# Optimization experiments

Measured on AMD Instinct MI355X. Metric: run time of the kernel, lower is better.

The kernel has to match this reference:

```python
import jax, jax.numpy as jnp
import numpy as np

EPS = 1e-5

def sparse_up_add(x, W, in_idx, out_idx, gamma, beta, skip):
    # x: [N_in, Cin]; W: [K, Cin, Cout]; in_idx/out_idx: [K, P]; skip: [N_out, Cout]
    n_out, c_out = skip.shape
    g = x[in_idx]                                   # [K, P, Cin] gather
    contrib = jnp.einsum('kpi,kio->kpo', g, W)      # [K, P, Cout] GEMM
    out = jnp.zeros((n_out, c_out), x.dtype)
    out = out.at[out_idx.reshape(-1)].add(contrib.reshape(-1, c_out))  # scatter-add
    # BatchNorm1d (training mode: batch stats over active voxels)
    mean = out.mean(axis=0)
    var = out.var(axis=0)
    y = (out - mean) * jax.lax.rsqrt(var + EPS) * gamma + beta
    return y + skip


def setup_inputs() -> dict:
    key = jax.random.key(0)
    ks = jax.random.split(key, 20)
    N3, N2, N1, N0 = 40000, 160000, 640000, 2560000
    C3, C2, C1 = 128, 64, 32
    K = 9
    d = {}
    d['x3'] = jax.random.normal(ks[0], (N3, C3), jnp.float32)
    d['skip3'] = jax.random.normal(ks[1], (N2, C2), jnp.float32)
    d['skip2'] = jax.random.normal(ks[2], (N1, C1), jnp.float32)
    d['skip1'] = jax.random.normal(ks[3], (N0, C1), jnp.float32)
    d['W3'] = jax.random.normal(ks[4], (K, C3, C2), jnp.float32) * (1.0 / np.sqrt(C3 * K))
    d['W2'] = jax.random.normal(ks[5], (K, C2, C1), jnp.float32) * (1.0 / np.sqrt(C2 * K))
    d['W1'] = jax.random.normal(ks[6], (K, C1, C1), jnp.float32) * (1.0 / np.sqrt(C1 * K))
    d['gamma3'] = jnp.ones((C2,), jnp.float32); d['beta3'] = jnp.zeros((C2,), jnp.float32)
    d['gamma2'] = jnp.ones((C1,), jnp.float32); d['beta2'] = jnp.zeros((C1,), jnp.float32)
    d['gamma1'] = jnp.ones((C1,), jnp.float32); d['beta1'] = jnp.zeros((C1,), jnp.float32)
    d['in_idx3'] = jax.random.randint(ks[7], (K, N3), 0, N3, jnp.int32)
    d['out_idx3'] = jax.random.randint(ks[8], (K, N3), 0, N2, jnp.int32)
    d['in_idx2'] = jax.random.randint(ks[9], (K, N2), 0, N2, jnp.int32)
    d['out_idx2'] = jax.random.randint(ks[10], (K, N2), 0, N1, jnp.int32)
    d['in_idx1'] = jax.random.randint(ks[11], (K, N1), 0, N1, jnp.int32)
    d['out_idx1'] = jax.random.randint(ks[12], (K, N1), 0, N0, jnp.int32)
    return d


def reference(x3, skip3, skip2, skip1, W3, W2, W1, gamma3, beta3, gamma2, beta2, gamma1, beta1,
              in_idx3, out_idx3, in_idx2, out_idx2, in_idx1, out_idx1):
    x = sparse_up_add(x3, W3, in_idx3, out_idx3, gamma3, beta3, skip3)  # up_3
    x = sparse_up_add(x, W2, in_idx2, out_idx2, gamma2, beta2, skip2)   # up_2
    x = sparse_up_add(x, W1, in_idx1, out_idx1, gamma1, beta1, skip1)   # up_1
    return x
```

## Files before the change

kernel.cpp:

```cpp
#include <hip/hip_runtime.h>

#define EPS 1e-5f

template <int CIN, int COUT, int RPB>
__global__ __launch_bounds__(256) void scatter_gemm_wreg(
    const float* __restrict__ x, const float* __restrict__ W,
    const int* __restrict__ in_idx, const int* __restrict__ out_idx,
    float* __restrict__ out, int P)
{
    const int GROUPS = 256 / COUT;
    const int k = blockIdx.y;
    const int o = threadIdx.x % COUT;
    const int g = threadIdx.x / COUT;

    float wcol[CIN];
    const float* __restrict__ Wk = W + (size_t)k * CIN * COUT + o;
#pragma unroll
    for (int i = 0; i < CIN; ++i) wcol[i] = Wk[(size_t)i * COUT];

    const int p0 = blockIdx.x * RPB;
    const int p1 = (p0 + RPB < P) ? (p0 + RPB) : P;
    const int rbase = k * P;

    for (int p = p0 + g; p < p1; p += GROUPS) {
        const int r = rbase + p;
        const int in   = in_idx[r];
        const int orow = out_idx[r];
        const float4* __restrict__ xr4 = (const float4*)(x + (size_t)in * CIN);
        float acc = 0.f;
#pragma unroll
        for (int i4 = 0; i4 < CIN / 4; ++i4) {
            const float4 xv = xr4[i4];
            acc = fmaf(xv.x, wcol[4 * i4 + 0], acc);
            acc = fmaf(xv.y, wcol[4 * i4 + 1], acc);
            acc = fmaf(xv.z, wcol[4 * i4 + 2], acc);
            acc = fmaf(xv.w, wcol[4 * i4 + 3], acc);
        }
        atomicAdd(&out[(size_t)orow * COUT + o], acc);
    }
}

template <int CIN, int RPB>
__global__ __launch_bounds__(256) void scatter_gemm_h2(
    const float* __restrict__ x, const float* __restrict__ W,
    const int* __restrict__ in_idx, const int* __restrict__ out_idx,
    float* __restrict__ out, int P)
{
    const int COUT = 32;
    const int HC = CIN / 2;
    const int WAVES = 256 / 64;
    const int k = blockIdx.y;
    const int lane = threadIdx.x & 63;
    const int w = threadIdx.x >> 6;
    const int o = lane & 31;
    const int h = lane >> 5;

    float wcol[HC];
    const float* __restrict__ Wk =
        W + (size_t)k * CIN * COUT + (size_t)h * HC * COUT + o;
#pragma unroll
    for (int i = 0; i < HC; ++i) wcol[i] = Wk[(size_t)i * COUT];

    const int p0 = blockIdx.x * RPB;
    const int p1 = (p0 + RPB < P) ? (p0 + RPB) : P;
    const int rbase = k * P;

    for (int p = p0 + w; p < p1; p += WAVES) {
        const int r = rbase + p;
        const int in   = in_idx[r];
        const int orow = out_idx[r];
        const float4* __restrict__ xr4 =
            (const float4*)(x + (size_t)in * CIN + h * HC);
        float acc = 0.f;
#pragma unroll
        for (int i4 = 0; i4 < HC / 4; ++i4) {
            const float4 xv = xr4[i4];
            acc = fmaf(xv.x, wcol[4 * i4 + 0], acc);
            acc = fmaf(xv.y, wcol[4 * i4 + 1], acc);
            acc = fmaf(xv.z, wcol[4 * i4 + 2], acc);
            acc = fmaf(xv.w, wcol[4 * i4 + 3], acc);
        }
        acc += __shfl_xor(acc, 32);
        if (h == 0) atomicAdd(&out[(size_t)orow * COUT + o], acc);
    }
}

template <int RPB>
__global__ __launch_bounds__(256) void scatter_gemm_l3_h2(
    const float* __restrict__ x, const float* __restrict__ W,
    const int* __restrict__ in_idx, const int* __restrict__ out_idx,
    float* __restrict__ out, int P)
{
    const int CIN = 128, COUT = 64;
    const int lane2 = threadIdx.x & 127;
    const int rg = threadIdx.x >> 7;
    const int o = lane2 & 63;
    const int h = lane2 >> 6;
    const int k = blockIdx.y;

    float wcol[64];
    const float* __restrict__ Wk =
        W + (size_t)k * CIN * COUT + (size_t)h * 64 * COUT + o;
#pragma unroll
    for (int i = 0; i < 64; ++i) wcol[i] = Wk[(size_t)i * COUT];

    __shared__ float part[2][64];

    const int p0 = blockIdx.x * RPB;
    const int rbase = k * P;

    for (int it = 0; it < RPB / 2; ++it) {
        const int p = p0 + it * 2 + rg;
        const int r = rbase + p;
        const int in   = in_idx[r];
        const int orow = out_idx[r];
        const float4* __restrict__ xr4 =
            (const float4*)(x + (size_t)in * CIN + h * 64);
        float acc = 0.f;
#pragma unroll
        for (int i4 = 0; i4 < 16; ++i4) {
            const float4 xv = xr4[i4];
            acc = fmaf(xv.x, wcol[4 * i4 + 0], acc);
            acc = fmaf(xv.y, wcol[4 * i4 + 1], acc);
            acc = fmaf(xv.z, wcol[4 * i4 + 2], acc);
            acc = fmaf(xv.w, wcol[4 * i4 + 3], acc);
        }
        if (h == 1) part[rg][o] = acc;
        __syncthreads();
        if (h == 0) {
            acc += part[rg][o];
            atomicAdd(&out[(size_t)orow * COUT + o], acc);
        }
        __syncthreads();
    }
}

template <int COUT>
__global__ __launch_bounds__(256) void reduce_stats(
    const float* __restrict__ out, float* __restrict__ stats, int n_rows)
{
    const int RPP = 256 / COUT;
    int c = threadIdx.x % COUT;
    float s = 0.f, ss = 0.f;
    int g = threadIdx.x / COUT;
    for (long long row = (long long)blockIdx.x * RPP + g; row < n_rows;
         row += (long long)gridDim.x * RPP) {
        float v = out[row * COUT + c];
        s += v;
        ss += v * v;
    }
    __shared__ float sh_s[256];
    __shared__ float sh_ss[256];
    sh_s[threadIdx.x] = s;
    sh_ss[threadIdx.x] = ss;
    __syncthreads();
    for (int off = 128; off >= COUT; off >>= 1) {
        if (threadIdx.x < off) {
            sh_s[threadIdx.x] += sh_s[threadIdx.x + off];
            sh_ss[threadIdx.x] += sh_ss[threadIdx.x + off];
        }
        __syncthreads();
    }
    if (threadIdx.x < COUT) {
        atomicAdd(&stats[c], sh_s[c]);
        atomicAdd(&stats[COUT + c], sh_ss[c]);
    }
}

template <int COUT>
__global__ __launch_bounds__(256) void bn_skip(
    float* __restrict__ out, const float* __restrict__ skip,
    const float* __restrict__ gamma, const float* __restrict__ beta,
    const float* __restrict__ stats, int n_rows)
{
    const int C4 = COUT / 4;
    long long idx = (long long)blockIdx.x * blockDim.x + threadIdx.x;
    long long total = (long long)n_rows * C4;
    if (idx >= total) return;
    int c4 = (int)(idx % C4);
    float4 v = ((const float4*)out)[idx];
    float4 sk = ((const float4*)skip)[idx];
    float inv_n = 1.f / (float)n_rows;
    float r[4] = {v.x, v.y, v.z, v.w};
    float skv[4] = {sk.x, sk.y, sk.z, sk.w};
#pragma unroll
    for (int j = 0; j < 4; ++j) {
        int c = c4 * 4 + j;
        float mean = stats[c] * inv_n;
        float var = stats[COUT + c] * inv_n - mean * mean;
        float scale = rsqrtf(var + EPS) * gamma[c];
        r[j] = (r[j] - mean) * scale + beta[c] + skv[j];
    }
    float4 res = {r[0], r[1], r[2], r[3]};
    ((float4*)out)[idx] = res;
}

extern "C" void kernel_launch(void* const* d_in, const int* in_sizes, int n_in,
                              void* d_out, int out_size, void* d_ws, size_t ws_size,
                              hipStream_t stream) {
    const float* x3    = (const float*)d_in[0];
    const float* skip3 = (const float*)d_in[1];
    const float* skip2 = (const float*)d_in[2];
    const float* skip1 = (const float*)d_in[3];
    const float* W3    = (const float*)d_in[4];
    const float* W2    = (const float*)d_in[5];
    const float* W1    = (const float*)d_in[6];
    const float* gamma3 = (const float*)d_in[7];
    const float* beta3  = (const float*)d_in[8];
    const float* gamma2 = (const float*)d_in[9];
    const float* beta2  = (const float*)d_in[10];
    const float* gamma1 = (const float*)d_in[11];
    const float* beta1  = (const float*)d_in[12];
    const int* in_idx3  = (const int*)d_in[13];
    const int* out_idx3 = (const int*)d_in[14];
    const int* in_idx2  = (const int*)d_in[15];
    const int* out_idx2 = (const int*)d_in[16];
    const int* in_idx1  = (const int*)d_in[17];
    const int* out_idx1 = (const int*)d_in[18];

    const int N3 = 40000, N2 = 160000, N1 = 640000, N0 = 2560000;
    const int K = 9;

    float* buf3  = (float*)d_ws;
    float* buf2  = buf3 + (size_t)N2 * 64;
    float* stats = buf2 + (size_t)N1 * 32;

    float* outp = (float*)d_out;

    hipMemsetAsync(buf3, 0, (size_t)N2 * 64 * sizeof(float), stream);
    hipMemsetAsync(stats, 0, 128 * sizeof(float), stream);
    {
        const int RPB = 16;
        dim3 grid(N3 / RPB, K);
        scatter_gemm_l3_h2<RPB><<<grid, 256, 0, stream>>>(
            x3, W3, in_idx3, out_idx3, buf3, N3);
    }
    reduce_stats<64><<<1024, 256, 0, stream>>>(buf3, stats, N2);
    {
        long long tot = (long long)N2 * (64 / 4);
        bn_skip<64><<<(int)((tot + 255) / 256), 256, 0, stream>>>(
            buf3, skip3, gamma3, beta3, stats, N2);
    }

    hipMemsetAsync(buf2, 0, (size_t)N1 * 32 * sizeof(float), stream);
    hipMemsetAsync(stats, 0, 128 * sizeof(float), stream);
    {
        const int RPB = 32;
        dim3 grid(N2 / RPB, K);
        scatter_gemm_h2<64, RPB><<<grid, 256, 0, stream>>>(
            buf3, W2, in_idx2, out_idx2, buf2, N2);
    }
    reduce_stats<32><<<2048, 256, 0, stream>>>(buf2, stats, N1);
    {
        long long tot = (long long)N1 * (32 / 4);
        bn_skip<32><<<(int)((tot + 255) / 256), 256, 0, stream>>>(
            buf2, skip2, gamma2, beta2, stats, N1);
    }

    hipMemsetAsync(outp, 0, (size_t)N0 * 32 * sizeof(float), stream);
    hipMemsetAsync(stats, 0, 128 * sizeof(float), stream);
    {
        const int RPB = 64;
        dim3 grid((N1 + RPB - 1) / RPB, K);
        scatter_gemm_wreg<32, 32, RPB><<<grid, 256, 0, stream>>>(
            buf2, W1, in_idx1, out_idx1, outp, N1);
    }
    reduce_stats<32><<<4096, 256, 0, stream>>>(outp, stats, N0);
    {
        long long tot = (long long)N0 * (32 / 4);
        bn_skip<32><<<(int)((tot + 255) / 256), 256, 0, stream>>>(
            outp, skip1, gamma1, beta1, stats, N0);
    }
}
```

Before: 2.947 ms.

## Unroll scatter-GEMM rows by two, split accumulators, drop LDS sync in layer 3

```diff
diff --git a/kernel.cpp b/kernel.cpp
--- a/kernel.cpp
+++ b/kernel.cpp
@@ -3,12 +3,13 @@
 #define EPS 1e-5f
 
 template <int CIN, int COUT, int RPB>
-__global__ __launch_bounds__(256) void scatter_gemm_wreg(
+__global__ __launch_bounds__(256, 8) void scatter_gemm_wreg2(
     const float* __restrict__ x, const float* __restrict__ W,
     const int* __restrict__ in_idx, const int* __restrict__ out_idx,
     float* __restrict__ out, int P)
 {
     const int GROUPS = 256 / COUT;
+    const int ITERS = RPB / GROUPS;
     const int k = blockIdx.y;
     const int o = threadIdx.x % COUT;
     const int g = threadIdx.x / COUT;
@@ -18,37 +19,47 @@
 #pragma unroll
     for (int i = 0; i < CIN; ++i) wcol[i] = Wk[(size_t)i * COUT];
 
-    const int p0 = blockIdx.x * RPB;
-    const int p1 = (p0 + RPB < P) ? (p0 + RPB) : P;
-    const int rbase = k * P;
-
-    for (int p = p0 + g; p < p1; p += GROUPS) {
-        const int r = rbase + p;
-        const int in   = in_idx[r];
-        const int orow = out_idx[r];
-        const float4* __restrict__ xr4 = (const float4*)(x + (size_t)in * CIN);
-        float acc = 0.f;
+    const int rbase = k * P + blockIdx.x * RPB + g;
+
+    for (int it = 0; it < ITERS; it += 2) {
+        const int r0 = rbase + it * GROUPS;
+        const int r1 = r0 + GROUPS;
+        const int in0 = in_idx[r0];
+        const int or0 = out_idx[r0];
+        const int in1 = in_idx[r1];
+        const int or1 = out_idx[r1];
+        const float4* __restrict__ a4 = (const float4*)(x + (size_t)in0 * CIN);
+        const float4* __restrict__ b4 = (const float4*)(x + (size_t)in1 * CIN);
+        float aa0 = 0.f, aa1 = 0.f, aa2 = 0.f, aa3 = 0.f;
+        float ba0 = 0.f, ba1 = 0.f, ba2 = 0.f, ba3 = 0.f;
 #pragma unroll
         for (int i4 = 0; i4 < CIN / 4; ++i4) {
-            const float4 xv = xr4[i4];
-            acc = fmaf(xv.x, wcol[4 * i4 + 0], acc);
-            acc = fmaf(xv.y, wcol[4 * i4 + 1], acc);
-            acc = fmaf(xv.z, wcol[4 * i4 + 2], acc);
-            acc = fmaf(xv.w, wcol[4 * i4 + 3], acc);
-        }
-        atomicAdd(&out[(size_t)orow * COUT + o], acc);
+            const float4 av = a4[i4];
+            const float4 bv = b4[i4];
+            aa0 = fmaf(av.x, wcol[4 * i4 + 0], aa0);
+            aa1 = fmaf(av.y, wcol[4 * i4 + 1], aa1);
+            aa2 = fmaf(av.z, wcol[4 * i4 + 2], aa2);
+            aa3 = fmaf(av.w, wcol[4 * i4 + 3], aa3);
+            ba0 = fmaf(bv.x, wcol[4 * i4 + 0], ba0);
+            ba1 = fmaf(bv.y, wcol[4 * i4 + 1], ba1);
+            ba2 = fmaf(bv.z, wcol[4 * i4 + 2], ba2);
+            ba3 = fmaf(bv.w, wcol[4 * i4 + 3], ba3);
+        }
+        atomicAdd(&out[(size_t)or0 * COUT + o], (aa0 + aa1) + (aa2 + aa3));
+        atomicAdd(&out[(size_t)or1 * COUT + o], (ba0 + ba1) + (ba2 + ba3));
     }
 }
 
 template <int CIN, int RPB>
-__global__ __launch_bounds__(256) void scatter_gemm_h2(
+__global__ __launch_bounds__(256, 8) void scatter_gemm_h2u(
     const float* __restrict__ x, const float* __restrict__ W,
     const int* __restrict__ in_idx, const int* __restrict__ out_idx,
     float* __restrict__ out, int P)
 {
     const int COUT = 32;
     const int HC = CIN / 2;
-    const int WAVES = 256 / 64;
+    const int WAVES = 4;
+    const int ITERS = RPB / WAVES;
     const int k = blockIdx.y;
     const int lane = threadIdx.x & 63;
     const int w = threadIdx.x >> 6;
@@ -61,77 +72,82 @@
 #pragma unroll
     for (int i = 0; i < HC; ++i) wcol[i] = Wk[(size_t)i * COUT];
 
-    const int p0 = blockIdx.x * RPB;
-    const int p1 = (p0 + RPB < P) ? (p0 + RPB) : P;
-    const int rbase = k * P;
-
-    for (int p = p0 + w; p < p1; p += WAVES) {
-        const int r = rbase + p;
-        const int in   = in_idx[r];
-        const int orow = out_idx[r];
-        const float4* __restrict__ xr4 =
-            (const float4*)(x + (size_t)in * CIN + h * HC);
-        float acc = 0.f;
+    const int rbase = k * P + blockIdx.x * RPB + w;
+
+    for (int it = 0; it < ITERS; it += 2) {
+        const int r0 = rbase + it * WAVES;
+        const int r1 = r0 + WAVES;
+        const int in0 = in_idx[r0];
+        const int or0 = out_idx[r0];
+        const int in1 = in_idx[r1];
+        const int or1 = out_idx[r1];
+        const float4* __restrict__ a4 =
+            (const float4*)(x + (size_t)in0 * CIN + h * HC);
+        const float4* __restrict__ b4 =
+            (const float4*)(x + (size_t)in1 * CIN + h * HC);
+        float aa0 = 0.f, aa1 = 0.f;
+        float ba0 = 0.f, ba1 = 0.f;
 #pragma unroll
         for (int i4 = 0; i4 < HC / 4; ++i4) {
-            const float4 xv = xr4[i4];
-            acc = fmaf(xv.x, wcol[4 * i4 + 0], acc);
-            acc = fmaf(xv.y, wcol[4 * i4 + 1], acc);
-            acc = fmaf(xv.z, wcol[4 * i4 + 2], acc);
-            acc = fmaf(xv.w, wcol[4 * i4 + 3], acc);
-        }
-        acc += __shfl_xor(acc, 32);
-        if (h == 0) atomicAdd(&out[(size_t)orow * COUT + o], acc);
+            const float4 av = a4[i4];
+            const float4 bv = b4[i4];
+            aa0 = fmaf(av.x, wcol[4 * i4 + 0], aa0);
+            aa1 = fmaf(av.y, wcol[4 * i4 + 1], aa1);
+            aa0 = fmaf(av.z, wcol[4 * i4 + 2], aa0);
+            aa1 = fmaf(av.w, wcol[4 * i4 + 3], aa1);
+            ba0 = fmaf(bv.x, wcol[4 * i4 + 0], ba0);
+            ba1 = fmaf(bv.y, wcol[4 * i4 + 1], ba1);
+            ba0 = fmaf(bv.z, wcol[4 * i4 + 2], ba0);
+            ba1 = fmaf(bv.w, wcol[4 * i4 + 3], ba1);
+        }
+        float acc0 = aa0 + aa1;
+        float acc1 = ba0 + ba1;
+        acc0 += __shfl_xor(acc0, 32);
+        acc1 += __shfl_xor(acc1, 32);
+        if (h == 0) {
+            atomicAdd(&out[(size_t)or0 * COUT + o], acc0);
+            atomicAdd(&out[(size_t)or1 * COUT + o], acc1);
+        }
     }
 }
 
 template <int RPB>
-__global__ __launch_bounds__(256) void scatter_gemm_l3_h2(
+__global__ __launch_bounds__(256, 4) void scatter_gemm_l3w(
     const float* __restrict__ x, const float* __restrict__ W,
     const int* __restrict__ in_idx, const int* __restrict__ out_idx,
     float* __restrict__ out, int P)
 {
     const int CIN = 128, COUT = 64;
-    const int lane2 = threadIdx.x & 127;
-    const int rg = threadIdx.x >> 7;
-    const int o = lane2 & 63;
-    const int h = lane2 >> 6;
+    const int w = threadIdx.x >> 6;
+    const int o = threadIdx.x & 63;
+    const int rp = w >> 1;
+    const int h = w & 1;
     const int k = blockIdx.y;
 
     float wcol[64];
     const float* __restrict__ Wk =
-        W + (size_t)k * CIN * COUT + (size_t)h * 64 * COUT + o;
+        W + (size_t)k * CIN * COUT + (size_t)(h * 64) * COUT + o;
 #pragma unroll
     for (int i = 0; i < 64; ++i) wcol[i] = Wk[(size_t)i * COUT];
 
-    __shared__ float part[2][64];
-
-    const int p0 = blockIdx.x * RPB;
-    const int rbase = k * P;
+    const int rbase = k * P + blockIdx.x * RPB + rp;
 
     for (int it = 0; it < RPB / 2; ++it) {
-        const int p = p0 + it * 2 + rg;
-        const int r = rbase + p;
-        const int in   = in_idx[r];
+        const int r = rbase + it * 2;
+        const int in = in_idx[r];
         const int orow = out_idx[r];
         const float4* __restrict__ xr4 =
             (const float4*)(x + (size_t)in * CIN + h * 64);
-        float acc = 0.f;
+        float a0 = 0.f, a1 = 0.f, a2 = 0.f, a3 = 0.f;
 #pragma unroll
         for (int i4 = 0; i4 < 16; ++i4) {
             const float4 xv = xr4[i4];
-            acc = fmaf(xv.x, wcol[4 * i4 + 0], acc);
-            acc = fmaf(xv.y, wcol[4 * i4 + 1], acc);
-            acc = fmaf(xv.z, wcol[4 * i4 + 2], acc);
-            acc = fmaf(xv.w, wcol[4 * i4 + 3], acc);
-        }
-        if (h == 1) part[rg][o] = acc;
-        __syncthreads();
-        if (h == 0) {
-            acc += part[rg][o];
-            atomicAdd(&out[(size_t)orow * COUT + o], acc);
-        }
-        __syncthreads();
+            a0 = fmaf(xv.x, wcol[4 * i4 + 0], a0);
+            a1 = fmaf(xv.y, wcol[4 * i4 + 1], a1);
+            a2 = fmaf(xv.z, wcol[4 * i4 + 2], a2);
+            a3 = fmaf(xv.w, wcol[4 * i4 + 3], a3);
+        }
+        atomicAdd(&out[(size_t)orow * COUT + o], (a0 + a1) + (a2 + a3));
     }
 }
 
@@ -232,7 +248,7 @@
     {
         const int RPB = 16;
         dim3 grid(N3 / RPB, K);
-        scatter_gemm_l3_h2<RPB><<<grid, 256, 0, stream>>>(
+        scatter_gemm_l3w<RPB><<<grid, 256, 0, stream>>>(
             x3, W3, in_idx3, out_idx3, buf3, N3);
     }
     reduce_stats<64><<<1024, 256, 0, stream>>>(buf3, stats, N2);
@@ -247,7 +263,7 @@
     {
         const int RPB = 32;
         dim3 grid(N2 / RPB, K);
-        scatter_gemm_h2<64, RPB><<<grid, 256, 0, stream>>>(
+        scatter_gemm_h2u<64, RPB><<<grid, 256, 0, stream>>>(
             buf3, W2, in_idx2, out_idx2, buf2, N2);
     }
     reduce_stats<32><<<2048, 256, 0, stream>>>(buf2, stats, N1);
@@ -261,8 +277,8 @@
     hipMemsetAsync(stats, 0, 128 * sizeof(float), stream);
     {
         const int RPB = 64;
-        dim3 grid((N1 + RPB - 1) / RPB, K);
-        scatter_gemm_wreg<32, 32, RPB><<<grid, 256, 0, stream>>>(
+        dim3 grid(N1 / RPB, K);
+        scatter_gemm_wreg2<32, 32, RPB><<<grid, 256, 0, stream>>>(
             buf2, W1, in_idx1, out_idx1, outp, N1);
     }
     reduce_stats<32><<<4096, 256, 0, stream>>>(outp, stats, N0);
```

Result: slower. 3.286 ms (+11.5%).
